# Kernel tuning notes

Measured on AMD Instinct MI355X. Metric: run time of the kernel, lower is better.

Reference implementation:

```python
import jax, jax.numpy as jnp
import numpy as np

B, S, D, H = 8, 1500, 1024, 16
HD = D // H
DFF = 4 * D
EPS = 1e-5


def _xavier(key, shape):
    fan_in, fan_out = shape[1], shape[0]
    limit = float(np.sqrt(6.0 / (fan_in + fan_out)))
    return jax.random.uniform(key, shape, jnp.float32, -limit, limit)


def setup_inputs() -> dict:
    key = jax.random.key(0)
    ks = jax.random.split(key, 8)
    return {
        "hidden_states": jax.random.normal(ks[0], (B, S, D), jnp.float32),
        "Wq": _xavier(ks[1], (D, D)),
        "Wk": _xavier(ks[2], (D, D)),
        "Wv": _xavier(ks[3], (D, D)),
        "Wo": _xavier(ks[4], (D, D)),
        "W1": _xavier(ks[5], (DFF, D)),
        "b1": jnp.zeros((DFF,), jnp.float32),
        "W2": _xavier(ks[6], (D, DFF)),
        "b2": jnp.zeros((D,), jnp.float32),
        "ln1_g": jnp.ones((D,), jnp.float32),
        "ln1_b": jnp.zeros((D,), jnp.float32),
        "ln2_g": jnp.ones((D,), jnp.float32),
        "ln2_b": jnp.zeros((D,), jnp.float32),
    }


def _layernorm(x, g, b):
    mu = jnp.mean(x, axis=-1, keepdims=True)
    var = jnp.mean(jnp.square(x - mu), axis=-1, keepdims=True)
    return (x - mu) * jax.lax.rsqrt(var + EPS) * g + b


def reference(hidden_states, Wq, Wk, Wv, Wo, W1, b1, W2, b2, ln1_g, ln1_b, ln2_g, ln2_b):
    x = hidden_states
    residual = x
    h = _layernorm(x, ln1_g, ln1_b)
    # torch Linear: y = h @ W.T ; reshape to heads
    q = (h @ Wq.T).reshape(B, S, H, HD).transpose(0, 2, 1, 3) * (HD ** -0.5)
    k = (h @ Wk.T).reshape(B, S, H, HD).transpose(0, 2, 1, 3)
    v = (h @ Wv.T).reshape(B, S, H, HD).transpose(0, 2, 1, 3)
    scores = jnp.einsum('bhqd,bhkd->bhqk', q, k)
    attn = jax.nn.softmax(scores.astype(jnp.float32), axis=-1).astype(h.dtype)
    ctx = jnp.einsum('bhqk,bhkd->bhqd', attn, v)
    ctx = ctx.transpose(0, 2, 1, 3).reshape(B, S, D)
    x = residual + ctx @ Wo.T
    residual = x
    h = _layernorm(x, ln2_g, ln2_b)
    ffn = jax.nn.gelu(h @ W1.T + b1, approximate=False) @ W2.T + b2
    return residual + ffn
```

## Files before the change

### kernel.cpp

```cpp
#include <hip/hip_runtime.h>
#include <hip/hip_bf16.h>
#include <cstdint>
#include <cstddef>

#define B_    8
#define S_    1500
#define D_    1024
#define H_    16
#define HD_   64
#define DFF_  4096
#define M_    12000
#define VTS_  1536

typedef __bf16 bf16;
typedef __attribute__((ext_vector_type(8))) __bf16 bf16x8;
typedef __attribute__((ext_vector_type(4))) float f32x4;

#define MFMA16(a, b, c) __builtin_amdgcn_mfma_f32_16x16x32_bf16((a), (b), (c), 0, 0, 0)

#define BAR()   do { __builtin_amdgcn_s_barrier(); __builtin_amdgcn_sched_barrier(0); } while (0)
#define LGKM0() do { asm volatile("s_waitcnt lgkmcnt(0)" ::: "memory"); __builtin_amdgcn_sched_barrier(0); } while (0)

static __device__ __forceinline__ void gload16(const void* g, void* l) {
  __builtin_amdgcn_global_load_lds(
      (const __attribute__((address_space(1))) void*)(uintptr_t)g,
      (__attribute__((address_space(3))) void*)(uintptr_t)l, 16, 0, 0);
}

static __device__ __forceinline__ unsigned short f2bu(float v) {
  bf16 h = (bf16)v;
  union { bf16 h; unsigned short u; } c;
  c.h = h;
  return c.u;
}

static constexpr size_t HSZ      = (size_t)M_ * D_ * 2;
static constexpr size_t H_OFF    = 0;
static constexpr size_t WQ_OFF   = H_OFF + HSZ;
static constexpr size_t WK_OFF   = WQ_OFF + (size_t)D_ * D_ * 2;
static constexpr size_t WV_OFF   = WK_OFF + (size_t)D_ * D_ * 2;
static constexpr size_t WO_OFF   = WV_OFF + (size_t)D_ * D_ * 2;
static constexpr size_t Q_OFF    = WO_OFF + (size_t)D_ * D_ * 2;
static constexpr size_t K_OFF    = Q_OFF + HSZ;
static constexpr size_t VT_OFF   = K_OFF + HSZ;
static constexpr size_t W1_OFF   = VT_OFF + (size_t)128 * 64 * VTS_ * 2;
static constexpr size_t W2_OFF   = W1_OFF + (size_t)DFF_ * D_ * 2;
static constexpr size_t WS_BASE  = W2_OFF + (size_t)DFF_ * D_ * 2;
static constexpr size_t H2B_OFF  = WS_BASE;
static constexpr size_t NEED_BIG = WS_BASE + HSZ;
static constexpr size_t H2F_OFF  = VT_OFF;
static constexpr size_t ACT_OFF  = 0;

__launch_bounds__(256)
__global__ void cvt_bf16(const float* __restrict__ src, bf16* __restrict__ dst, int n) {
  int i = (blockIdx.x * 256 + threadIdx.x) * 4;
  if (i < n) {
    float4 f = *(const float4*)(src + i);
    dst[i + 0] = (bf16)f.x;
    dst[i + 1] = (bf16)f.y;
    dst[i + 2] = (bf16)f.z;
    dst[i + 3] = (bf16)f.w;
  }
}

__launch_bounds__(256)
__global__ void ln_fused(const float* __restrict__ x, const float* __restrict__ g,
                         const float* __restrict__ bb, bf16* __restrict__ out) {
  const int row = blockIdx.x;
  const int t = threadIdx.x;
  const float4 xv = *(const float4*)(x + (size_t)row * D_ + t * 4);
  float s  = xv.x + xv.y + xv.z + xv.w;
  float s2 = xv.x * xv.x + xv.y * xv.y + xv.z * xv.z + xv.w * xv.w;
#pragma unroll
  for (int m = 32; m >= 1; m >>= 1) {
    s  += __shfl_xor(s, m);
    s2 += __shfl_xor(s2, m);
  }
  __shared__ float red[8];
  const int w = t >> 6;
  if ((t & 63) == 0) { red[w] = s; red[4 + w] = s2; }
  __syncthreads();
  s  = red[0] + red[1] + red[2] + red[3];
  s2 = red[4] + red[5] + red[6] + red[7];
  const float mu  = s * (1.0f / D_);
  const float var = s2 * (1.0f / D_) - mu * mu;
  const float rs  = rsqrtf(var + 1e-5f);
  const float4 gv = *(const float4*)(g + t * 4);
  const float4 bv = *(const float4*)(bb + t * 4);
  bf16* o = out + (size_t)row * D_ + t * 4;
  o[0] = (bf16)((xv.x - mu) * rs * gv.x + bv.x);
  o[1] = (bf16)((xv.y - mu) * rs * gv.y + bv.y);
  o[2] = (bf16)((xv.z - mu) * rs * gv.z + bv.z);
  o[3] = (bf16)((xv.w - mu) * rs * gv.w + bv.w);
}

template <int EPI>
__launch_bounds__(512, 2)
__global__ void gemm256(const bf16* __restrict__ A, const bf16* __restrict__ Bw,
                        int M, int N, int K,
                        bf16* __restrict__ outB, float* outF,
                        const float* __restrict__ bias, const float* resid,
                        bf16* __restrict__ outQ, bf16* __restrict__ outK2,
                        bf16* __restrict__ outV) {
  __shared__ bf16 a_lds[4][256 * 32];
  __shared__ bf16 b_lds[4][256 * 32];

  const int t = threadIdx.x;
  const int lane = t & 63, wid = t >> 6;
  const int wm = wid >> 2, wn = wid & 3;
  const int l15 = lane & 15, hi = lane >> 4;
  const int mrow0 = blockIdx.x * 256;
  const int ncol0 = blockIdx.y * 256;

  const int pc = hi ^ ((l15 >> 1) & 3);

  const int s0 = t, s1 = 512 + t;
  const int ar0 = s0 >> 2, ar1 = s1 >> 2;
  const int ac0 = ((s0 & 3) ^ ((ar0 >> 1) & 3)) * 8;
  const int ac1 = ((s1 & 3) ^ ((ar1 >> 1) & 3)) * 8;
  int ga0 = mrow0 + ar0; ga0 = ga0 < M ? ga0 : M - 1;
  int ga1 = mrow0 + ar1; ga1 = ga1 < M ? ga1 : M - 1;
  const bf16* a0 = A + (size_t)ga0 * K + ac0;
  const bf16* a1 = A + (size_t)ga1 * K + ac1;
  const bf16* b0 = Bw + (size_t)(ncol0 + ar0) * K + ac0;
  const bf16* b1 = Bw + (size_t)(ncol0 + ar1) * K + ac1;

  f32x4 acc[8][4] = {};

  const int NT = K >> 5;

  gload16(a0,      (char*)&a_lds[0][0] + s0 * 16);
  gload16(a1,      (char*)&a_lds[0][0] + s1 * 16);
  gload16(b0,      (char*)&b_lds[0][0] + s0 * 16);
  gload16(b1,      (char*)&b_lds[0][0] + s1 * 16);
  gload16(a0 + 32, (char*)&a_lds[1][0] + s0 * 16);
  gload16(a1 + 32, (char*)&a_lds[1][0] + s1 * 16);
  gload16(b0 + 32, (char*)&b_lds[1][0] + s0 * 16);
  gload16(b1 + 32, (char*)&b_lds[1][0] + s1 * 16);
  asm volatile("s_waitcnt vmcnt(4)" ::: "memory");
  BAR();

  int buf = 0;
  for (int tt = 0; tt < NT; ++tt) {
    const bf16* al = &a_lds[buf][0];
    const bf16* bl = &b_lds[buf][0];
    const bool do_stage = (tt + 2) < NT;
    const int nb = (tt + 2) & 3;
    const int k2 = (tt + 2) << 5;

    if (do_stage) {
      gload16(a0 + k2, (char*)&a_lds[nb][0] + s0 * 16);
      gload16(a1 + k2, (char*)&a_lds[nb][0] + s1 * 16);
    }
    bf16x8 bf_[4], af_[4];
#pragma unroll
    for (int n = 0; n < 4; ++n)
      bf_[n] = *(const bf16x8*)&bl[(wn * 64 + n * 16 + l15) * 32 + pc * 8];
#pragma unroll
    for (int m = 0; m < 4; ++m)
      af_[m] = *(const bf16x8*)&al[(wm * 128 + m * 16 + l15) * 32 + pc * 8];
    BAR();
    LGKM0();
    __builtin_amdgcn_s_setprio(1);
#pragma unroll
    for (int m = 0; m < 4; ++m)
#pragma unroll
      for (int n = 0; n < 4; ++n)
        acc[m][n] = MFMA16(af_[m], bf_[n], acc[m][n]);
    __builtin_amdgcn_s_setprio(0);
    BAR();

    if (do_stage) {
      gload16(b0 + k2, (char*)&b_lds[nb][0] + s0 * 16);
      gload16(b1 + k2, (char*)&b_lds[nb][0] + s1 * 16);
    }
#pragma unroll
    for (int m = 0; m < 4; ++m)
      af_[m] = *(const bf16x8*)&al[(wm * 128 + (m + 4) * 16 + l15) * 32 + pc * 8];
    BAR();
    LGKM0();
    __builtin_amdgcn_s_setprio(1);
#pragma unroll
    for (int m = 0; m < 4; ++m)
#pragma unroll
      for (int n = 0; n < 4; ++n)
        acc[m + 4][n] = MFMA16(af_[m], bf_[n], acc[m + 4][n]);
    __builtin_amdgcn_s_setprio(0);
    if (do_stage) asm volatile("s_waitcnt vmcnt(4)" ::: "memory");
    else          asm volatile("s_waitcnt vmcnt(0)" ::: "memory");
    BAR();
    buf = (buf + 1) & 3;
  }

  const int r0 = hi * 4;

  if constexpr (EPI == 5) {
    const int mm = blockIdx.y >> 2;
    const int nloc0 = (blockIdx.y & 3) * 256;
    if (mm == 2) {
#pragma unroll
      for (int m = 0; m < 8; ++m) {
        int row0 = mrow0 + wm * 128 + m * 16 + r0;
        if (row0 < M) {
          int bb2 = row0 / 1500;
          int s = row0 - bb2 * 1500;
#pragma unroll
          for (int n = 0; n < 4; ++n) {
            int f = nloc0 + wn * 64 + n * 16 + l15;
            size_t a = ((size_t)(bb2 * 16 + (f >> 6)) * 64 + (f & 63)) * VTS_ + s;
            ushort4 pk;
            pk.x = f2bu(acc[m][n][0]);
            pk.y = f2bu(acc[m][n][1]);
            pk.z = f2bu(acc[m][n][2]);
            pk.w = f2bu(acc[m][n][3]);
            *reinterpret_cast<ushort4*>((unsigned short*)outV + a) = pk;
          }
        }
      }
    } else {
      bf16* dst = (mm == 0) ? outQ : outK2;
      const float sc = (mm == 0) ? 0.125f : 1.0f;
#pragma unroll
      for (int m = 0; m < 8; ++m) {
#pragma unroll
        for (int n = 0; n < 4; ++n) {
          int col = nloc0 + wn * 64 + n * 16 + l15;
#pragma unroll
          for (int r = 0; r < 4; ++r) {
            int row = mrow0 + wm * 128 + m * 16 + r0 + r;
            if (row < M) dst[(size_t)row * D_ + col] = (bf16)(acc[m][n][r] * sc);
          }
        }
      }
    }
    return;
  }

#pragma unroll
  for (int m = 0; m < 8; ++m) {
#pragma unroll
    for (int n = 0; n < 4; ++n) {
      int col = ncol0 + wn * 64 + n * 16 + l15;
#pragma unroll
      for (int r = 0; r < 4; ++r) {
        int row = mrow0 + wm * 128 + m * 16 + r0 + r;
        if (row < M) {
          float v = acc[m][n][r];
          if constexpr (EPI == 2) {
            float xg = v + bias[col];
            v = 0.5f * xg * (1.0f + erff(xg * 0.70710678118654752f));
            outB[(size_t)row * N + col] = (bf16)v;
          }
          if constexpr (EPI == 3) {
            v += resid[(size_t)row * N + col];
            if (bias) v += bias[col];
            outF[(size_t)row * N + col] = v;
          }
        }
      }
    }
  }
}

template <int EPI>
__launch_bounds__(256)
__global__ void gemm_bt(const bf16* __restrict__ A, const bf16* __restrict__ Bw,
                        int M, int N, int K,
                        bf16* __restrict__ outB, float* outF,
                        const float* __restrict__ bias, const float* resid,
                        float scale) {
  __shared__ bf16 a_lds[128 * 64];
  __shared__ bf16 b_lds[128 * 64];
  const int t = threadIdx.x;
  const int lane = t & 63, wid = t >> 6;
  const int wr = wid >> 1, wc = wid & 1;
  const int mrow0 = blockIdx.x * 128;
  const int ncol0 = blockIdx.y * 128;
  const int l15 = lane & 15;
  const int khi = (lane >> 4) << 3;

  f32x4 acc[4][4] = {};

  for (int k0 = 0; k0 < K; k0 += 64) {
#pragma unroll
    for (int i = 0; i < 4; ++i) {
      int idx = i * 2048 + t * 8;
      int row = idx >> 6, col = idx & 63;
      int gr = mrow0 + row;
      gr = gr < M ? gr : M - 1;
      gload16(A + (size_t)gr * K + (k0 + col), (char*)a_lds + idx * 2);
    }
#pragma unroll
    for (int i = 0; i < 4; ++i) {
      int idx = i * 2048 + t * 8;
      int row = idx >> 6, col = idx & 63;
      gload16(Bw + (size_t)(ncol0 + row) * K + (k0 + col), (char*)b_lds + idx * 2);
    }
    __syncthreads();
#pragma unroll
    for (int kk = 0; kk < 2; ++kk) {
      bf16x8 af[4], bfv[4];
#pragma unroll
      for (int m = 0; m < 4; ++m)
        af[m] = *(const bf16x8*)&a_lds[(wr * 64 + m * 16 + l15) * 64 + kk * 32 + khi];
#pragma unroll
      for (int n = 0; n < 4; ++n)
        bfv[n] = *(const bf16x8*)&b_lds[(wc * 64 + n * 16 + l15) * 64 + kk * 32 + khi];
#pragma unroll
      for (int m = 0; m < 4; ++m)
#pragma unroll
        for (int n = 0; n < 4; ++n)
          acc[m][n] = MFMA16(af[m], bfv[n], acc[m][n]);
    }
    __syncthreads();
  }

  const int r0 = (lane >> 4) << 2;
#pragma unroll
  for (int m = 0; m < 4; ++m) {
#pragma unroll
    for (int n = 0; n < 4; ++n) {
      int col = ncol0 + wc * 64 + n * 16 + l15;
#pragma unroll
      for (int r = 0; r < 4; ++r) {
        int row = mrow0 + wr * 64 + m * 16 + r0 + r;
        if (row < M) {
          float v = acc[m][n][r];
          if constexpr (EPI == 2) {
            float xg = v + bias[col];
            v = 0.5f * xg * (1.0f + erff(xg * 0.70710678118654752f));
          }
          if constexpr (EPI == 3) {
            v += resid[(size_t)row * N + col];
            if (bias) v += bias[col];
            outF[(size_t)row * N + col] = v;
          } else {
            outB[(size_t)row * N + col] = (bf16)v;
          }
        }
      }
    }
  }
}

__launch_bounds__(256, 4)
__global__ void attn_fwd5(const bf16* __restrict__ q, const bf16* __restrict__ kg,
                          const bf16* __restrict__ vt, bf16* __restrict__ cx) {
  __shared__ bf16 k_lds[2][64 * 64];
  __shared__ bf16 v_lds[2][64 * 64];
  __shared__ bf16 p_lds[4][16 * 64];

  const int t = threadIdx.x;
  const int lane = t & 63, w = t >> 6;
  const int qt = blockIdx.x;
  const int bh = blockIdx.y;
  const int l15 = lane & 15;
  const int hi = lane >> 4;
  const int khi = hi << 3;

  const size_t hoff = ((size_t)(bh >> 4) * S_) * D_ + (size_t)(bh & 15) * HD_;
  const bf16* qh = q + hoff;
  const bf16* kh = kg + hoff;
  const bf16* vh = vt + (size_t)bh * (64 * VTS_);

  const int st_r0 = t >> 3;
  const int st_c  = t & 7;

  int qr = qt * 64 + w * 16 + l15;
  int qrc = qr < S_ ? qr : S_ - 1;
  const bf16x8 qf0 = *(const bf16x8*)(qh + (size_t)qrc * D_ + khi);
  const bf16x8 qf1 = *(const bf16x8*)(qh + (size_t)qrc * D_ + 32 + khi);

  f32x4 oacc[4] = {};
  float mrun[4], lrun[4];
#pragma unroll
  for (int r = 0; r < 4; ++r) { mrun[r] = -1e30f; lrun[r] = 0.f; }

  bf16* pw = &p_lds[w][0];
  const int NT = (S_ + 63) / 64;

#pragma unroll
  for (int i = 0; i < 2; ++i) {
    int row = i * 32 + st_r0;
    int sc = st_c ^ (row & 7);
    int key = row < S_ ? row : S_ - 1;
    gload16(kh + (size_t)key * D_ + sc * 8, (char*)&k_lds[0][0] + (i * 2048 + t * 8) * 2);
    gload16(vh + (size_t)row * VTS_ + sc * 8, (char*)&v_lds[0][0] + (i * 2048 + t * 8) * 2);
  }
  __syncthreads();

  int buf = 0;
  for (int kt = 0; kt < NT; ++kt) {
    if (kt + 1 < NT) {
      int kb = (kt + 1) * 64;
#pragma unroll
      for (int i = 0; i < 2; ++i) {
        int row = i * 32 + st_r0;
        int sc = st_c ^ (row & 7);
        int key = kb + row;
        key = key < S_ ? key : S_ - 1;
        gload16(kh + (size_t)key * D_ + sc * 8,
                (char*)&k_lds[buf ^ 1][0] + (i * 2048 + t * 8) * 2);
        gload16(vh + (size_t)row * VTS_ + kb + sc * 8,
                (char*)&v_lds[buf ^ 1][0] + (i * 2048 + t * 8) * 2);
      }
    }

    float pv[4][4];
#pragma unroll
    for (int nb = 0; nb < 4; ++nb) {
      int krow = nb * 16 + l15;
      f32x4 z = {};
      z = MFMA16(qf0, *(const bf16x8*)&k_lds[buf][krow * 64 + ((hi ^ (l15 & 7)) << 3)], z);
      z = MFMA16(qf1, *(const bf16x8*)&k_lds[buf][krow * 64 + (((4 + hi) ^ (l15 & 7)) << 3)], z);
      int key = kt * 64 + krow;
      bool cvld = key < S_;
#pragma unroll
      for (int r = 0; r < 4; ++r) pv[nb][r] = cvld ? z[r] : -1e30f;
    }

    float mx4[4];
#pragma unroll
    for (int r = 0; r < 4; ++r) {
      float mx = fmaxf(fmaxf(pv[0][r], pv[1][r]), fmaxf(pv[2][r], pv[3][r]));
      mx = fmaxf(mx, __shfl_xor(mx, 1));
      mx = fmaxf(mx, __shfl_xor(mx, 2));
      mx = fmaxf(mx, __shfl_xor(mx, 4));
      mx = fmaxf(mx, __shfl_xor(mx, 8));
      mx4[r] = mx;
    }

    bool ok = (mx4[0] <= mrun[0] + 8.f) && (mx4[1] <= mrun[1] + 8.f) &&
              (mx4[2] <= mrun[2] + 8.f) && (mx4[3] <= mrun[3] + 8.f);
    if (!__all(ok)) {
#pragma unroll
      for (int r = 0; r < 4; ++r) {
        float mnew = fmaxf(mrun[r], mx4[r]);
        float corr = __expf(mrun[r] - mnew);
        lrun[r] *= corr;
        mrun[r] = mnew;
#pragma unroll
        for (int db = 0; db < 4; ++db) oacc[db][r] *= corr;
      }
    }

#pragma unroll
    for (int r = 0; r < 4; ++r) {
      float ps = 0.f;
#pragma unroll
      for (int nb = 0; nb < 4; ++nb) {
        float p = __expf(pv[nb][r] - mrun[r]);
        pv[nb][r] = p;
        ps += p;
      }
      ps += __shfl_xor(ps, 1);
      ps += __shfl_xor(ps, 2);
      ps += __shfl_xor(ps, 4);
      ps += __shfl_xor(ps, 8);
      lrun[r] += ps;
    }

#pragma unroll
    for (int nb = 0; nb < 4; ++nb) {
#pragma unroll
      for (int r = 0; r < 4; ++r) {
        int prow = hi * 4 + r;
        int pcol = (nb * 16 + l15) ^ ((prow & 7) << 3);
        pw[prow * 64 + pcol] = (bf16)pv[nb][r];
      }
    }

#pragma unroll
    for (int kk = 0; kk < 2; ++kk) {
      bf16x8 pf = *(const bf16x8*)&pw[l15 * 64 + (((kk * 4 + hi) ^ (l15 & 7)) << 3)];
#pragma unroll
      for (int db = 0; db < 4; ++db) {
        int vrow = db * 16 + l15;
        bf16x8 vf = *(const bf16x8*)&v_lds[buf][vrow * 64 + (((kk * 4 + hi) ^ (l15 & 7)) << 3)];
        oacc[db] = MFMA16(pf, vf, oacc[db]);
      }
    }

    __syncthreads();
    buf ^= 1;
  }

#pragma unroll
  for (int r = 0; r < 4; ++r) {
    int qrow = qt * 64 + w * 16 + hi * 4 + r;
    if (qrow < S_) {
      float inv = 1.0f / lrun[r];
#pragma unroll
      for (int db = 0; db < 4; ++db)
        cx[hoff + (size_t)qrow * D_ + db * 16 + l15] = (bf16)(oacc[db][r] * inv);
    }
  }
}

extern "C" void kernel_launch(void* const* d_in, const int* in_sizes, int n_in,
                              void* d_out, int out_size, void* d_ws, size_t ws_size,
                              hipStream_t stream) {
  const float* x   = (const float*)d_in[0];
  const float* Wq  = (const float*)d_in[1];
  const float* Wk  = (const float*)d_in[2];
  const float* Wv  = (const float*)d_in[3];
  const float* Wo  = (const float*)d_in[4];
  const float* W1  = (const float*)d_in[5];
  const float* b1  = (const float*)d_in[6];
  const float* W2  = (const float*)d_in[7];
  const float* b2  = (const float*)d_in[8];
  const float* g1  = (const float*)d_in[9];
  const float* be1 = (const float*)d_in[10];
  const float* g2  = (const float*)d_in[11];
  const float* be2 = (const float*)d_in[12];
  float* out = (float*)d_out;

  char* ws = (char*)d_ws;
  bf16* h_b   = (bf16*)(ws + H_OFF);
  bf16* wq_b  = (bf16*)(ws + WQ_OFF);
  bf16* wk_b  = (bf16*)(ws + WK_OFF);
  bf16* wv_b  = (bf16*)(ws + WV_OFF);
  bf16* wo_b  = (bf16*)(ws + WO_OFF);
  bf16* w1_b  = (bf16*)(ws + W1_OFF);
  bf16* w2_b  = (bf16*)(ws + W2_OFF);
  bf16* q_b   = (bf16*)(ws + Q_OFF);
  bf16* k_b   = (bf16*)(ws + K_OFF);
  bf16* vt_b  = (bf16*)(ws + VT_OFF);
  bf16* act_b = (bf16*)(ws + ACT_OFF);
  bf16* ctx_b = h_b;

  const bool big = ws_size >= NEED_BIG;
  bf16* h2_b = (bf16*)(ws + (big ? H2B_OFF : H2F_OFF));

  cvt_bf16<<<(D_ * D_) / 1024, 256, 0, stream>>>(Wq, wq_b, D_ * D_);
  cvt_bf16<<<(D_ * D_) / 1024, 256, 0, stream>>>(Wk, wk_b, D_ * D_);
  cvt_bf16<<<(D_ * D_) / 1024, 256, 0, stream>>>(Wv, wv_b, D_ * D_);
  cvt_bf16<<<(D_ * D_) / 1024, 256, 0, stream>>>(Wo, wo_b, D_ * D_);
  cvt_bf16<<<(DFF_ * D_) / 1024, 256, 0, stream>>>(W1, w1_b, DFF_ * D_);
  cvt_bf16<<<(DFF_ * D_) / 1024, 256, 0, stream>>>(W2, w2_b, DFF_ * D_);

  ln_fused<<<M_, 256, 0, stream>>>(x, g1, be1, h_b);

  gemm256<5><<<dim3((M_ + 255) / 256, 12), 512, 0, stream>>>(
      h_b, wq_b, M_, 3072, D_, nullptr, nullptr, nullptr, nullptr, q_b, k_b, vt_b);

  attn_fwd5<<<dim3((S_ + 63) / 64, B_ * H_), 256, 0, stream>>>(q_b, k_b, vt_b, ctx_b);

  gemm256<3><<<dim3((M_ + 255) / 256, 4), 512, 0, stream>>>(
      ctx_b, wo_b, M_, D_, D_, nullptr, out, nullptr, x, nullptr, nullptr, nullptr);

  ln_fused<<<M_, 256, 0, stream>>>(out, g2, be2, h2_b);

  if (big) {
    gemm256<2><<<dim3((M_ + 255) / 256, DFF_ / 256), 512, 0, stream>>>(
        h2_b, w1_b, M_, DFF_, D_, act_b, nullptr, b1, nullptr,
        nullptr, nullptr, nullptr);
    gemm256<3><<<dim3((M_ + 255) / 256, D_ / 256), 512, 0, stream>>>(
        act_b, w2_b, M_, D_, DFF_, nullptr, out, b2, out,
        nullptr, nullptr, nullptr);
  } else {
    for (int c = 0; c < 3; ++c) {
      int r0c = c * 4000;
      int nr = 4000;
      gemm256<2><<<dim3((nr + 255) / 256, DFF_ / 256), 512, 0, stream>>>(
          h2_b + (size_t)r0c * D_, w1_b, nr, DFF_, D_, act_b, nullptr, b1, nullptr,
          nullptr, nullptr, nullptr);
      gemm_bt<3><<<dim3((nr + 127) / 128, D_ / 128), 256, 0, stream>>>(
          act_b, w2_b, nr, D_, DFF_, nullptr, out + (size_t)r0c * D_, b2,
          out + (size_t)r0c * D_, 0.f);
    }
  }
}
```

Before: 787.8 us.

## Use exp2 softmax with log2e-folded Q scale, lazy row reductions, and XCD-aware remap

Folds log2(e) into the Q scaling so the attention softmax can use exp2f. The row max shuffle-reduction now runs only when a rescale is needed, the per-tile row-sum shuffle is deferred to the epilogue, and padding masking is limited to the last key tile. It also adds s_setprio around the MFMA sections and remaps a 1D grid so consecutive blocks spread across the 8 XCDs. Lazy rescaling with a per-lane local max means thresholds differ per lane, which slightly changes numerics.

```diff
diff --git a/kernel.cpp b/kernel.cpp
--- a/kernel.cpp
+++ b/kernel.cpp
@@ -219,7 +219,7 @@
       }
     } else {
       bf16* dst = (mm == 0) ? outQ : outK2;
-      const float sc = (mm == 0) ? 0.125f : 1.0f;
+      const float sc = (mm == 0) ? 0.18033688011112042f : 1.0f;
 #pragma unroll
       for (int m = 0; m < 8; ++m) {
 #pragma unroll
@@ -344,7 +344,7 @@
 }
 
 __launch_bounds__(256, 4)
-__global__ void attn_fwd5(const bf16* __restrict__ q, const bf16* __restrict__ kg,
+__global__ void attn_fwd6(const bf16* __restrict__ q, const bf16* __restrict__ kg,
                           const bf16* __restrict__ vt, bf16* __restrict__ cx) {
   __shared__ bf16 k_lds[2][64 * 64];
   __shared__ bf16 v_lds[2][64 * 64];
@@ -352,8 +352,10 @@
 
   const int t = threadIdx.x;
   const int lane = t & 63, w = t >> 6;
-  const int qt = blockIdx.x;
-  const int bh = blockIdx.y;
+  const int L = blockIdx.x;
+  const int wu = (L & 7) * 384 + (L >> 3);
+  const int bh = wu / 24;
+  const int qt = wu - bh * 24;
   const int l15 = lane & 15;
   const int hi = lane >> 4;
   const int khi = hi << 3;
@@ -378,6 +380,7 @@
 
   bf16* pw = &p_lds[w][0];
   const int NT = (S_ + 63) / 64;
+  const float THR = 11.5415605f;
 
 #pragma unroll
   for (int i = 0; i < 2; ++i) {
@@ -407,36 +410,44 @@
     }
 
     float pv[4][4];
+    __builtin_amdgcn_s_setprio(1);
 #pragma unroll
     for (int nb = 0; nb < 4; ++nb) {
       int krow = nb * 16 + l15;
       f32x4 z = {};
       z = MFMA16(qf0, *(const bf16x8*)&k_lds[buf][krow * 64 + ((hi ^ (l15 & 7)) << 3)], z);
       z = MFMA16(qf1, *(const bf16x8*)&k_lds[buf][krow * 64 + (((4 + hi) ^ (l15 & 7)) << 3)], z);
-      int key = kt * 64 + krow;
-      bool cvld = key < S_;
-#pragma unroll
-      for (int r = 0; r < 4; ++r) pv[nb][r] = cvld ? z[r] : -1e30f;
-    }
-
-    float mx4[4];
+#pragma unroll
+      for (int r = 0; r < 4; ++r) pv[nb][r] = z[r];
+    }
+    __builtin_amdgcn_s_setprio(0);
+
+    if (kt == NT - 1) {
+#pragma unroll
+      for (int nb = 0; nb < 4; ++nb) {
+        bool cvld = (kt * 64 + nb * 16 + l15) < S_;
+#pragma unroll
+        for (int r = 0; r < 4; ++r) pv[nb][r] = cvld ? pv[nb][r] : -1e30f;
+      }
+    }
+
+    float lmax[4];
+    bool ok = true;
 #pragma unroll
     for (int r = 0; r < 4; ++r) {
-      float mx = fmaxf(fmaxf(pv[0][r], pv[1][r]), fmaxf(pv[2][r], pv[3][r]));
-      mx = fmaxf(mx, __shfl_xor(mx, 1));
-      mx = fmaxf(mx, __shfl_xor(mx, 2));
-      mx = fmaxf(mx, __shfl_xor(mx, 4));
-      mx = fmaxf(mx, __shfl_xor(mx, 8));
-      mx4[r] = mx;
-    }
-
-    bool ok = (mx4[0] <= mrun[0] + 8.f) && (mx4[1] <= mrun[1] + 8.f) &&
-              (mx4[2] <= mrun[2] + 8.f) && (mx4[3] <= mrun[3] + 8.f);
+      lmax[r] = fmaxf(fmaxf(pv[0][r], pv[1][r]), fmaxf(pv[2][r], pv[3][r]));
+      ok = ok && (lmax[r] <= mrun[r] + THR);
+    }
     if (!__all(ok)) {
 #pragma unroll
       for (int r = 0; r < 4; ++r) {
-        float mnew = fmaxf(mrun[r], mx4[r]);
-        float corr = __expf(mrun[r] - mnew);
+        float mx = lmax[r];
+        mx = fmaxf(mx, __shfl_xor(mx, 1));
+        mx = fmaxf(mx, __shfl_xor(mx, 2));
+        mx = fmaxf(mx, __shfl_xor(mx, 4));
+        mx = fmaxf(mx, __shfl_xor(mx, 8));
+        float mnew = fmaxf(mrun[r], mx);
+        float corr = exp2f(mrun[r] - mnew);
         lrun[r] *= corr;
         mrun[r] = mnew;
 #pragma unroll
@@ -446,18 +457,12 @@
 
 #pragma unroll
     for (int r = 0; r < 4; ++r) {
-      float ps = 0.f;
-#pragma unroll
-      for (int nb = 0; nb < 4; ++nb) {
-        float p = __expf(pv[nb][r] - mrun[r]);
-        pv[nb][r] = p;
-        ps += p;
-      }
-      ps += __shfl_xor(ps, 1);
-      ps += __shfl_xor(ps, 2);
-      ps += __shfl_xor(ps, 4);
-      ps += __shfl_xor(ps, 8);
-      lrun[r] += ps;
+      float p0 = exp2f(pv[0][r] - mrun[r]);
+      float p1 = exp2f(pv[1][r] - mrun[r]);
+      float p2 = exp2f(pv[2][r] - mrun[r]);
+      float p3 = exp2f(pv[3][r] - mrun[r]);
+      pv[0][r] = p0; pv[1][r] = p1; pv[2][r] = p2; pv[3][r] = p3;
+      lrun[r] += (p0 + p1) + (p2 + p3);
     }
 
 #pragma unroll
@@ -470,6 +475,7 @@
       }
     }
 
+    __builtin_amdgcn_s_setprio(1);
 #pragma unroll
     for (int kk = 0; kk < 2; ++kk) {
       bf16x8 pf = *(const bf16x8*)&pw[l15 * 64 + (((kk * 4 + hi) ^ (l15 & 7)) << 3)];
@@ -480,6 +486,7 @@
         oacc[db] = MFMA16(pf, vf, oacc[db]);
       }
     }
+    __builtin_amdgcn_s_setprio(0);
 
     __syncthreads();
     buf ^= 1;
@@ -487,9 +494,14 @@
 
 #pragma unroll
   for (int r = 0; r < 4; ++r) {
+    float ps = lrun[r];
+    ps += __shfl_xor(ps, 1);
+    ps += __shfl_xor(ps, 2);
+    ps += __shfl_xor(ps, 4);
+    ps += __shfl_xor(ps, 8);
     int qrow = qt * 64 + w * 16 + hi * 4 + r;
     if (qrow < S_) {
-      float inv = 1.0f / lrun[r];
+      float inv = 1.0f / ps;
 #pragma unroll
       for (int db = 0; db < 4; ++db)
         cx[hoff + (size_t)qrow * D_ + db * 16 + l15] = (bf16)(oacc[db][r] * inv);
@@ -544,7 +556,7 @@
   gemm256<5><<<dim3((M_ + 255) / 256, 12), 512, 0, stream>>>(
       h_b, wq_b, M_, 3072, D_, nullptr, nullptr, nullptr, nullptr, q_b, k_b, vt_b);
 
-  attn_fwd5<<<dim3((S_ + 63) / 64, B_ * H_), 256, 0, stream>>>(q_b, k_b, vt_b, ctx_b);
+  attn_fwd6<<<3072, 256, 0, stream>>>(q_b, k_b, vt_b, ctx_b);
 
   gemm256<3><<<dim3((M_ + 255) / 256, 4), 512, 0, stream>>>(
       ctx_b, wo_b, M_, D_, D_, nullptr, out, nullptr, x, nullptr, nullptr, nullptr);
```

Result: faster. 733.1 us (-7.0%).
